# Kernel optimization log

Measured on AMD Instinct MI355X. Metric: run time of the kernel, lower is better.

## Reference

```python
import jax, jax.numpy as jnp
import numpy as np
from jax import lax

D_MODEL = 512
CLASS_NUM = 8000
MAX_LEN = 80
VOCAB = 8002  # len(char2idx): chars + sos/eos
SOS_IDX = 0


def setup_inputs() -> dict:
    key = jax.random.key(0)
    ks = jax.random.split(key, 16)
    T, B, D, V, C = 128, 128, D_MODEL, VOCAB, CLASS_NUM
    s = 1.0 / np.sqrt(D)
    inp = {
        "inputs": jax.random.normal(ks[0], (T, B, D), jnp.float32),
        # additive attention params (query_size=key_size=hidden_size=D)
        "Wq": jax.random.normal(ks[1], (D, D), jnp.float32) * s,
        "bq": jnp.zeros((D,), jnp.float32),
        "Wk": jax.random.normal(ks[2], (D, D), jnp.float32) * s,
        "bk": jnp.zeros((D,), jnp.float32),
        "v": jax.random.normal(ks[3], (D,), jnp.float32) * s,
        # GRUCell: input_size = 2*D, hidden_size = D (PyTorch layout)
        "W_ih": jax.random.normal(ks[4], (3 * D, 2 * D), jnp.float32) * s,
        "b_ih": jnp.zeros((3 * D,), jnp.float32),
        "W_hh": jax.random.normal(ks[5], (3 * D, D), jnp.float32) * s,
        "b_hh": jnp.zeros((3 * D,), jnp.float32),
        # embedding table and classifier
        "emb": jax.random.normal(ks[6], (V, D), jnp.float32),
        "Wc": jax.random.normal(ks[7], (C, D), jnp.float32) * s,
        "bc": jnp.zeros((C,), jnp.float32),
    }
    return inp


def _gru_cell(x, h, W_ih, b_ih, W_hh, b_hh):
    # PyTorch GRUCell math
    gi = x @ W_ih.T + b_ih  # [B, 3D]
    gh = h @ W_hh.T + b_hh  # [B, 3D]
    i_r, i_z, i_n = jnp.split(gi, 3, axis=1)
    h_r, h_z, h_n = jnp.split(gh, 3, axis=1)
    r = jax.nn.sigmoid(i_r + h_r)
    z = jax.nn.sigmoid(i_z + h_z)
    n = jnp.tanh(i_n + r * h_n)
    return (1.0 - z) * n + z * h


def reference(inputs, Wq, bq, Wk, bk, v, W_ih, b_ih, W_hh, b_hh, emb, Wc, bc):
    T, B, D = inputs.shape
    # Attention is called as attention(inputs, keys) with keys = inputs each
    # step -> weights are loop-invariant; compute the context once.
    e = jnp.tanh(inputs @ Wq.T + bq + inputs @ Wk.T + bk) @ v  # [T, B]
    att = jax.nn.softmax(e, axis=0)[..., None]  # [T, B, 1]
    c = jnp.sum(att * inputs, axis=0)  # [B, D]

    h0 = inputs[0]  # initial GRU hidden = first encoder frame
    out0 = emb[jnp.full((B,), SOS_IDX, dtype=jnp.int32)]  # sos embedding

    def step(carry, _):
        h, out = carry
        x = jnp.concatenate([out, c], axis=1)  # [B, 2D]
        h = _gru_cell(x, h, W_ih, b_ih, W_hh, b_hh)
        pred = h @ Wc.T + bc  # [B, class_num]
        top1 = jnp.argmax(pred, axis=1)  # greedy decode (eval mode)
        return (h, emb[top1]), pred

    _, preds = lax.scan(step, (h0, out0), None, length=MAX_LEN)
    return preds  # [max_len, B, class_num]
```

## Files before the change

### kernel.cpp

```cpp
#include <hip/hip_runtime.h>
#include <cstdint>
#include <cstddef>

#define D_MOD 512
#define TH3   1536
#define CLS   8000
#define MAXLEN 80
#define B_SZ  128
#define T_LEN 128
#define NK0   16

typedef __attribute__((ext_vector_type(8))) __bf16 bf16x8;
typedef __attribute__((ext_vector_type(8))) unsigned short u16x8;
typedef __attribute__((ext_vector_type(4))) float f32x4;

__device__ __forceinline__ unsigned short f2bf(float x) {
    unsigned u = __float_as_uint(x);
    unsigned r = ((u >> 16) & 1u) + 0x7fffu;
    return (unsigned short)((u + r) >> 16);
}
__device__ __forceinline__ float bf2f(unsigned short h) {
    return __uint_as_float(((unsigned)h) << 16);
}
__device__ __forceinline__ f32x4 mfma16(u16x8 a, u16x8 b, f32x4 c) {
    return __builtin_amdgcn_mfma_f32_16x16x32_bf16(
        __builtin_bit_cast(bf16x8, a), __builtin_bit_cast(bf16x8, b), c, 0, 0, 0);
}
__device__ __forceinline__ void conv8(const float* __restrict__ p, u16x8& hi, u16x8& lo) {
    float4 f0 = *(const float4*)p;
    float4 f1 = *(const float4*)(p + 4);
    float fs[8] = {f0.x, f0.y, f0.z, f0.w, f1.x, f1.y, f1.z, f1.w};
    #pragma unroll
    for (int j = 0; j < 8; ++j) {
        unsigned short h = f2bf(fs[j]);
        hi[j] = h;
        lo[j] = f2bf(fs[j] - bf2f(h));
    }
}
__device__ __forceinline__ unsigned long long packkey(float v, int n) {
    unsigned u = __float_as_uint(v);
    u = (u & 0x80000000u) ? ~u : (u | 0x80000000u);
    return ((unsigned long long)u << 32) | (unsigned)(~(unsigned)n);
}
__device__ __forceinline__ unsigned long long shfl_xor_u64(unsigned long long x, int mask) {
    unsigned lo = (unsigned)x, hi = (unsigned)(x >> 32);
    lo = __shfl_xor(lo, mask, 16);
    hi = __shfl_xor(hi, mask, 16);
    return ((unsigned long long)hi << 32) | lo;
}
__device__ __forceinline__ size_t pk_off(int n, int k) {
    int tile = n >> 4, lr = n & 15, k0i = k >> 5, lk = (k >> 3) & 3, e = k & 7;
    return ((size_t)(tile * NK0 + k0i) * 64 + (lk * 16 + lr)) * 8 + e;
}

__global__ __launch_bounds__(256) void cvt2p_kernel(
    const float* __restrict__ s1, const float* __restrict__ s2, int ld,
    long total4, unsigned short* __restrict__ hi, unsigned short* __restrict__ lo)
{
    long i4 = (long)blockIdx.x * 256 + threadIdx.x;
    if (i4 >= total4) return;
    long r = i4 >> 7;
    int c = (int)(i4 & 127) * 4;
    float4 a = *(const float4*)(s1 + r * (long)ld + c);
    if (s2) {
        float4 b = *(const float4*)(s2 + r * (long)ld + c);
        a.x += b.x; a.y += b.y; a.z += b.z; a.w += b.w;
    }
    float xs[4] = {a.x, a.y, a.z, a.w};
    unsigned short hs[4], ls[4];
    #pragma unroll
    for (int j = 0; j < 4; ++j) {
        hs[j] = f2bf(xs[j]);
        ls[j] = f2bf(xs[j] - bf2f(hs[j]));
    }
    size_t o = pk_off((int)r, c);
    *(ushort4*)(hi + o) = make_ushort4(hs[0], hs[1], hs[2], hs[3]);
    *(ushort4*)(lo + o) = make_ushort4(ls[0], ls[1], ls[2], ls[3]);
}

template<bool GATHER_CONV, bool CONVB, bool ADD2D, bool ARGMAX, int NS, int KS>
__device__ __forceinline__ void gemm_ks2(
    const unsigned short* __restrict__ Ahi, const unsigned short* __restrict__ Alo,
    const float* __restrict__ Afp, const unsigned long long* __restrict__ gslot,
    const unsigned short* __restrict__ Bhi, const unsigned short* __restrict__ Blo,
    const float* __restrict__ Bfp,
    const float* __restrict__ bias, const float* __restrict__ D2,
    float* __restrict__ C, int ldc,
    unsigned long long* __restrict__ aslot, int bx, int by)
{
    static_assert(NS * KS == 8, "8 waves per block");
    __shared__ float red[(KS - 1) * NS * 576];
    const int tid = threadIdx.x;
    const int w = tid >> 6, lane = tid & 63;
    const int lr = lane & 15, lk = lane >> 4;
    const int ns = w % NS, ks = w / NS;
    const int m0 = by * 16;
    const int n0 = (bx * NS + ns) * 32;
    const int tA = by;
    const int tB0 = n0 >> 4, tB1 = tB0 + 1;

    const float* paf = nullptr;
    if constexpr (GATHER_CONV) {
        int g = (int)(~(unsigned)gslot[m0 + lr]);
        paf = Afp + (size_t)g * D_MOD + lk * 8;
    }
    const float *pb0f = nullptr, *pb1f = nullptr;
    if constexpr (CONVB) {
        pb0f = Bfp + (size_t)(n0 + lr) * D_MOD + lk * 8;
        pb1f = Bfp + (size_t)(n0 + 16 + lr) * D_MOD + lk * 8;
    }

    f32x4 acc0 = (f32x4){0.f, 0.f, 0.f, 0.f};
    f32x4 acc1 = (f32x4){0.f, 0.f, 0.f, 0.f};

    const int kBeg = ks * (NK0 / KS), kEnd = kBeg + (NK0 / KS);
    for (int k0i = kBeg; k0i < kEnd; ++k0i) {
        u16x8 ah, al, b0h, b0l, b1h, b1l;
        if constexpr (GATHER_CONV) {
            conv8(paf + k0i * 32, ah, al);
        } else {
            size_t oA = ((size_t)(tA * NK0 + k0i) * 64 + lane) * 8;
            ah = *(const u16x8*)(Ahi + oA); al = *(const u16x8*)(Alo + oA);
        }
        if constexpr (CONVB) {
            conv8(pb0f + k0i * 32, b0h, b0l);
            conv8(pb1f + k0i * 32, b1h, b1l);
        } else {
            size_t oB0 = ((size_t)(tB0 * NK0 + k0i) * 64 + lane) * 8;
            size_t oB1 = ((size_t)(tB1 * NK0 + k0i) * 64 + lane) * 8;
            b0h = *(const u16x8*)(Bhi + oB0); b0l = *(const u16x8*)(Blo + oB0);
            b1h = *(const u16x8*)(Bhi + oB1); b1l = *(const u16x8*)(Blo + oB1);
        }
        acc0 = mfma16(ah, b0h, acc0);
        acc0 = mfma16(ah, b0l, acc0);
        acc0 = mfma16(al, b0h, acc0);
        acc1 = mfma16(ah, b1h, acc1);
        acc1 = mfma16(ah, b1l, acc1);
        acc1 = mfma16(al, b1h, acc1);
    }

    float af[8];
    #pragma unroll
    for (int i = 0; i < 4; ++i) { af[i] = acc0[i]; af[4 + i] = acc1[i]; }

    if (ks > 0) {
        const int slot = (ks - 1) * NS + ns;
        #pragma unroll
        for (int i = 0; i < 8; ++i) red[slot * 576 + lane * 9 + i] = af[i];
    }
    __syncthreads();
    if (ks == 0) {
        #pragma unroll
        for (int j = 1; j < KS; ++j) {
            const int slot = (j - 1) * NS + ns;
            #pragma unroll
            for (int i = 0; i < 8; ++i) af[i] += red[slot * 576 + lane * 9 + i];
        }
        #pragma unroll
        for (int r = 0; r < 4; ++r) {
            const int row = m0 + lk * 4 + r;
            unsigned long long kmax = 0ull;
            #pragma unroll
            for (int ni = 0; ni < 2; ++ni) {
                const int col = n0 + ni * 16 + lr;
                float val = af[ni * 4 + r];
                if (bias) val += bias[col];
                if constexpr (ADD2D) val += D2[(size_t)row * ldc + col];
                C[(size_t)row * ldc + col] = val;
                if constexpr (ARGMAX) {
                    unsigned long long k = packkey(val, col);
                    if (k > kmax) kmax = k;
                }
            }
            if constexpr (ARGMAX) {
                #pragma unroll
                for (int off = 1; off < 16; off <<= 1) {
                    unsigned long long o = shfl_xor_u64(kmax, off);
                    if (o > kmax) kmax = o;
                }
                if (lr == 0) atomicMax(&aslot[row], kmax);
            }
        }
    }
}

template<int G>
__device__ __forceinline__ bool xcd_map(int p, int& bx, int& by) {
    int x = p & 7, s = p >> 3;
    by = s & 7;
    bx = x * G + (s >> 3);
    return true;
}

__global__ __launch_bounds__(512) void step_dual_kernel(
    const unsigned short* __restrict__ hHi, const unsigned short* __restrict__ hLo,
    const unsigned short* __restrict__ WhhHi, const unsigned short* __restrict__ WhhLo,
    const float* __restrict__ b_hh,
    const float* __restrict__ emb, const unsigned long long* __restrict__ sPrev,
    const unsigned short* __restrict__ WihaHi, const unsigned short* __restrict__ WihaLo,
    const float* __restrict__ gc,
    float* __restrict__ gh, float* __restrict__ gi)
{
    int p = blockIdx.x;
    const int z = (p >= 384);
    p -= z * 384;
    int bx, by;
    xcd_map<6>(p, bx, by);
    if (z == 0)
        gemm_ks2<false, false, false, false, 1, 8>(hHi, hLo, nullptr, nullptr,
            WhhHi, WhhLo, nullptr, b_hh, nullptr, gh, TH3, nullptr, bx, by);
    else
        gemm_ks2<true, false, true, false, 1, 8>(nullptr, nullptr, emb, sPrev,
            WihaHi, WihaLo, nullptr, nullptr, gc, gi, TH3, nullptr, bx, by);
}

__global__ __launch_bounds__(512) void gemm128_kernel(
    const unsigned short* __restrict__ Ahi, const unsigned short* __restrict__ Alo,
    const unsigned short* __restrict__ Bhi, const unsigned short* __restrict__ Blo,
    const float* __restrict__ bias, float* __restrict__ C)
{
    int bx, by;
    xcd_map<6>(blockIdx.x, bx, by);
    gemm_ks2<false, false, false, false, 1, 8>(Ahi, Alo, nullptr, nullptr,
        Bhi, Blo, nullptr, bias, nullptr, C, TH3, nullptr, bx, by);
}

template<bool CONVB>
__global__ __launch_bounds__(512) void cls_kernel(
    const unsigned short* __restrict__ hHi, const unsigned short* __restrict__ hLo,
    const unsigned short* __restrict__ WcHi, const unsigned short* __restrict__ WcLo,
    const float* __restrict__ Wc, const float* __restrict__ bc,
    float* __restrict__ C, unsigned long long* __restrict__ aslot)
{
    int bx, by;
    xcd_map<16>(blockIdx.x, bx, by);
    if (bx >= 125) return;
    gemm_ks2<false, CONVB, false, true, 2, 4>(hHi, hLo, nullptr, nullptr,
        WcHi, WcLo, Wc, bc, nullptr, C, CLS, aslot, bx, by);
}

__global__ __launch_bounds__(256) void attn_e_mfma(
    const float* __restrict__ inp,
    const unsigned short* __restrict__ WqkHi, const unsigned short* __restrict__ WqkLo,
    const float* __restrict__ bq, const float* __restrict__ bk,
    const float* __restrict__ v, float* __restrict__ e)
{
    __shared__ __align__(16) unsigned short Ah[32][40];
    __shared__ __align__(16) unsigned short Al[32][40];
    __shared__ float red[4][32];
    const int tid = threadIdx.x, w = tid >> 6, lane = tid & 63;
    const int lr = lane & 15, lk = lane >> 4;
    const int m0 = blockIdx.x * 32;
    const int srow = tid >> 3, scol = (tid & 7) * 4;

    f32x4 acc[2][8];
    #pragma unroll
    for (int i = 0; i < 2; ++i)
        #pragma unroll
        for (int j = 0; j < 8; ++j) acc[i][j] = (f32x4){0.f, 0.f, 0.f, 0.f};

    for (int k0i = 0; k0i < NK0; ++k0i) {
        float4 x = *(const float4*)(inp + (size_t)(m0 + srow) * D_MOD + k0i * 32 + scol);
        float xs[4] = {x.x, x.y, x.z, x.w};
        #pragma unroll
        for (int j = 0; j < 4; ++j) {
            unsigned short h = f2bf(xs[j]);
            Ah[srow][scol + j] = h;
            Al[srow][scol + j] = f2bf(xs[j] - bf2f(h));
        }
        __syncthreads();
        u16x8 a[2][2];
        #pragma unroll
        for (int mi = 0; mi < 2; ++mi) {
            a[mi][0] = *(const u16x8*)&Ah[mi * 16 + lr][lk * 8];
            a[mi][1] = *(const u16x8*)&Al[mi * 16 + lr][lk * 8];
        }
        #pragma unroll
        for (int nf = 0; nf < 8; ++nf) {
            const int tile = w * 8 + nf;
            size_t ob = ((size_t)(tile * NK0 + k0i) * 64 + lane) * 8;
            u16x8 bh = *(const u16x8*)(WqkHi + ob);
            u16x8 bl = *(const u16x8*)(WqkLo + ob);
            #pragma unroll
            for (int mi = 0; mi < 2; ++mi) {
                acc[mi][nf] = mfma16(a[mi][0], bh, acc[mi][nf]);
                acc[mi][nf] = mfma16(a[mi][0], bl, acc[mi][nf]);
                acc[mi][nf] = mfma16(a[mi][1], bh, acc[mi][nf]);
            }
        }
        __syncthreads();
    }

    float ep[2][4];
    #pragma unroll
    for (int mi = 0; mi < 2; ++mi)
        #pragma unroll
        for (int r = 0; r < 4; ++r) ep[mi][r] = 0.f;
    #pragma unroll
    for (int nf = 0; nf < 8; ++nf) {
        const int col = w * 128 + nf * 16 + lr;
        const float bb = bq[col] + bk[col];
        const float vv = v[col];
        #pragma unroll
        for (int mi = 0; mi < 2; ++mi)
            #pragma unroll
            for (int r = 0; r < 4; ++r)
                ep[mi][r] += vv * tanhf(acc[mi][nf][r] + bb);
    }
    #pragma unroll
    for (int mi = 0; mi < 2; ++mi)
        #pragma unroll
        for (int r = 0; r < 4; ++r) {
            float s = ep[mi][r];
            #pragma unroll
            for (int off = 1; off < 16; off <<= 1) s += __shfl_xor(s, off, 16);
            if (lr == 0) red[w][mi * 16 + lk * 4 + r] = s;
        }
    __syncthreads();
    if (tid < 32) e[m0 + tid] = red[0][tid] + red[1][tid] + red[2][tid] + red[3][tid];
}

__global__ __launch_bounds__(256) void softmax_ctx_kernel(
    const float* __restrict__ inp, const float* __restrict__ e,
    unsigned short* __restrict__ cHi, unsigned short* __restrict__ cLo,
    float* __restrict__ h1, unsigned short* __restrict__ h1Hi, unsigned short* __restrict__ h1Lo,
    unsigned long long* __restrict__ slots)
{
    __shared__ float att[T_LEN];
    __shared__ float red;
    const int b = blockIdx.x, tid = threadIdx.x;
    float val = -1e30f;
    if (tid < T_LEN) { val = e[(size_t)tid * B_SZ + b]; att[tid] = val; }
    __syncthreads();
    if (tid < 64) {
        float m = fmaxf(att[tid], att[tid + 64]);
        #pragma unroll
        for (int off = 32; off; off >>= 1) m = fmaxf(m, __shfl_xor(m, off));
        if (tid == 0) red = m;
    }
    __syncthreads();
    const float mx = red;
    __syncthreads();
    if (tid < T_LEN) att[tid] = expf(val - mx);
    __syncthreads();
    if (tid < 64) {
        float s = att[tid] + att[tid + 64];
        #pragma unroll
        for (int off = 32; off; off >>= 1) s += __shfl_xor(s, off);
        if (tid == 0) red = s;
    }
    __syncthreads();
    const float inv = 1.f / red;

    const int d0 = tid * 2;
    float ax = 0.f, ay = 0.f;
    for (int t = 0; t < T_LEN; ++t) {
        float a = att[t];
        float2 x = *(const float2*)(inp + ((size_t)t * B_SZ + b) * D_MOD + d0);
        ax += a * x.x; ay += a * x.y;
        if (t == 0) {
            *(float2*)(h1 + (size_t)b * D_MOD + d0) = x;
            unsigned short hx = f2bf(x.x), hy = f2bf(x.y);
            h1Hi[pk_off(b, d0)]     = hx;
            h1Hi[pk_off(b, d0 + 1)] = hy;
            h1Lo[pk_off(b, d0)]     = f2bf(x.x - bf2f(hx));
            h1Lo[pk_off(b, d0 + 1)] = f2bf(x.y - bf2f(hy));
        }
    }
    ax *= inv; ay *= inv;
    unsigned short cx = f2bf(ax), cy = f2bf(ay);
    cHi[pk_off(b, d0)]     = cx;
    cHi[pk_off(b, d0 + 1)] = cy;
    cLo[pk_off(b, d0)]     = f2bf(ax - bf2f(cx));
    cLo[pk_off(b, d0 + 1)] = f2bf(ay - bf2f(cy));
    if (tid == 0) {
        slots[b] = 0ull;
        slots[B_SZ + b] = 0x00000000FFFFFFFFull;
    }
}

__global__ __launch_bounds__(512) void gru_combine(
    const float* __restrict__ gh, const float* __restrict__ gi,
    const float* __restrict__ hPrev, float* __restrict__ hCur,
    unsigned short* __restrict__ hHiC, unsigned short* __restrict__ hLoC,
    unsigned long long* __restrict__ slotCur)
{
    const int b = blockIdx.x, k = threadIdx.x;
    const float* gib = gi + (size_t)b * TH3;
    const float* ghb = gh + (size_t)b * TH3;
    float r = 1.f / (1.f + expf(-(gib[k] + ghb[k])));
    float z = 1.f / (1.f + expf(-(gib[k + 512] + ghb[k + 512])));
    float n = tanhf(gib[k + 1024] + r * ghb[k + 1024]);
    float h = hPrev[(size_t)b * D_MOD + k];
    float hv = (1.f - z) * n + z * h;
    hCur[(size_t)b * D_MOD + k] = hv;
    unsigned short hh = f2bf(hv);
    size_t o = pk_off(b, k);
    hHiC[o] = hh;
    hLoC[o] = f2bf(hv - bf2f(hh));
    if (k == 0) slotCur[b] = 0ull;
}

extern "C" void kernel_launch(void* const* d_in, const int* in_sizes, int n_in,
                              void* d_out, int out_size, void* d_ws, size_t ws_size,
                              hipStream_t stream)
{
    const float* inp  = (const float*)d_in[0];
    const float* Wq   = (const float*)d_in[1];
    const float* bq   = (const float*)d_in[2];
    const float* Wk   = (const float*)d_in[3];
    const float* bk   = (const float*)d_in[4];
    const float* v    = (const float*)d_in[5];
    const float* W_ih = (const float*)d_in[6];
    const float* b_ih = (const float*)d_in[7];
    const float* W_hh = (const float*)d_in[8];
    const float* b_hh = (const float*)d_in[9];
    const float* emb  = (const float*)d_in[10];
    const float* Wc   = (const float*)d_in[11];
    const float* bc   = (const float*)d_in[12];
    float* out = (float*)d_out;

    char* base = (char*)d_ws;
    size_t off = 0;
    auto alloc = [&](size_t bytes) -> char* {
        char* q = base + off;
        off += (bytes + 255) & ~(size_t)255;
        return q;
    };
    typedef unsigned short us;
    us* WqkHi  = (us*)alloc(512 * 512 * 2);
    us* WqkLo  = (us*)alloc(512 * 512 * 2);
    us* WhhHi  = (us*)alloc((size_t)TH3 * 512 * 2);
    us* WhhLo  = (us*)alloc((size_t)TH3 * 512 * 2);
    us* WihaHi = (us*)alloc((size_t)TH3 * 512 * 2);
    us* WihaLo = (us*)alloc((size_t)TH3 * 512 * 2);
    us* WihbHi = (us*)alloc((size_t)TH3 * 512 * 2);
    us* WihbLo = (us*)alloc((size_t)TH3 * 512 * 2);
    float* e   = (float*)alloc(T_LEN * B_SZ * 4);
    us* cHi    = (us*)alloc(B_SZ * 512 * 2);
    us* cLo    = (us*)alloc(B_SZ * 512 * 2);
    float* gc  = (float*)alloc((size_t)B_SZ * TH3 * 4);
    float* gh  = (float*)alloc((size_t)B_SZ * TH3 * 4);
    float* gi  = (float*)alloc((size_t)B_SZ * TH3 * 4);
    float* hF[2]; us* hHi[2]; us* hLo[2];
    hF[0] = (float*)alloc(B_SZ * 512 * 4);
    hF[1] = (float*)alloc(B_SZ * 512 * 4);
    hHi[0] = (us*)alloc(B_SZ * 512 * 2);
    hHi[1] = (us*)alloc(B_SZ * 512 * 2);
    hLo[0] = (us*)alloc(B_SZ * 512 * 2);
    hLo[1] = (us*)alloc(B_SZ * 512 * 2);
    unsigned long long* slots = (unsigned long long*)alloc(2 * B_SZ * 8);
    us* WcHi = (us*)alloc((size_t)CLS * 512 * 2);
    us* WcLo = (us*)alloc((size_t)CLS * 512 * 2);
    const bool PREB = (off <= ws_size);

    cvt2p_kernel<<<(512 * 128) / 256, 256, 0, stream>>>(Wq, Wk, 512, 512L * 128, WqkHi, WqkLo);
    cvt2p_kernel<<<(TH3 * 128) / 256, 256, 0, stream>>>(W_hh, nullptr, 512, (long)TH3 * 128, WhhHi, WhhLo);
    cvt2p_kernel<<<(TH3 * 128) / 256, 256, 0, stream>>>(W_ih, nullptr, 1024, (long)TH3 * 128, WihaHi, WihaLo);
    cvt2p_kernel<<<(TH3 * 128) / 256, 256, 0, stream>>>(W_ih + 512, nullptr, 1024, (long)TH3 * 128, WihbHi, WihbLo);
    if (PREB)
        cvt2p_kernel<<<(CLS * 128) / 256, 256, 0, stream>>>(Wc, nullptr, 512, (long)CLS * 128, WcHi, WcLo);

    attn_e_mfma<<<(T_LEN * B_SZ) / 32, 256, 0, stream>>>(inp, WqkHi, WqkLo, bq, bk, v, e);
    softmax_ctx_kernel<<<B_SZ, 256, 0, stream>>>(inp, e, cHi, cLo, hF[1], hHi[1], hLo[1], slots);
    gemm128_kernel<<<384, 512, 0, stream>>>(cHi, cLo, WihbHi, WihbLo, b_ih, gc);

    for (int t = 0; t < MAXLEN; ++t) {
        const int pi = (t + 1) & 1, ci = t & 1;
        unsigned long long* sPrev = slots + pi * B_SZ;
        unsigned long long* sCur  = slots + ci * B_SZ;

        step_dual_kernel<<<768, 512, 0, stream>>>(
            hHi[pi], hLo[pi], WhhHi, WhhLo, b_hh,
            emb, sPrev, WihaHi, WihaLo, gc, gh, gi);
        gru_combine<<<B_SZ, 512, 0, stream>>>(
            gh, gi, hF[pi], hF[ci], hHi[ci], hLo[ci], sCur);
        if (PREB)
            cls_kernel<false><<<1024, 512, 0, stream>>>(
                hHi[ci], hLo[ci], WcHi, WcLo, nullptr, bc,
                out + (size_t)t * B_SZ * CLS, sCur);
        else
            cls_kernel<true><<<1024, 512, 0, stream>>>(
                hHi[ci], hLo[ci], nullptr, nullptr, Wc, bc,
                out + (size_t)t * B_SZ * CLS, sCur);
    }
}
```

Before: 2.986 ms.

## Precompute embedding input-gate table and fuse GRU combine into hidden GEMM

Greedy decoding only ever feeds embedding rows into the W_ih input half, so the code now computes emb @ W_ih_a once for all 8000 class rows before the loop. Each step then gathers the needed row instead of running a per-step gathered GEMM. The per-step gh GEMM kernel also absorbs the GRU elementwise update: the last 32 blocks to finish, detected with an atomic counter, spin until every block is done and then compute the new hidden state, which removes one launch per step. The trade-offs are a large one-time GEMM with a big fp32 table, and a grid-wide spin-wait that relies on all blocks being resident at the same time.

Result: slower. 4.045 ms (+35.5%).

```diff
diff --git a/kernel.cpp b/kernel.cpp
--- a/kernel.cpp
+++ b/kernel.cpp
@@ -9,6 +9,7 @@
 #define B_SZ  128
 #define T_LEN 128
 #define NK0   16
+#define EGI_ROWS 8000
 
 typedef __attribute__((ext_vector_type(8))) __bf16 bf16x8;
 typedef __attribute__((ext_vector_type(8))) unsigned short u16x8;
@@ -101,7 +102,7 @@
 
     const float* paf = nullptr;
     if constexpr (GATHER_CONV) {
-        int g = (int)(~(unsigned)gslot[m0 + lr]);
+        int g = gslot ? (int)(~(unsigned)gslot[m0 + lr]) : (m0 + lr);
         paf = Afp + (size_t)g * D_MOD + lk * 8;
     }
     const float *pb0f = nullptr, *pb1f = nullptr;
@@ -192,26 +193,80 @@
     return true;
 }
 
-__global__ __launch_bounds__(512) void step_dual_kernel(
+__global__ __launch_bounds__(512) void egi_kernel(
+    const float* __restrict__ emb,
+    const unsigned short* __restrict__ WihaHi, const unsigned short* __restrict__ WihaLo,
+    float* __restrict__ Egi)
+{
+    int p = blockIdx.x;
+    int x = p & 7, s = p >> 3;
+    int by = s % 500, bx = x * 6 + s / 500;
+    gemm_ks2<true, false, false, false, 1, 8>(nullptr, nullptr, emb, nullptr,
+        WihaHi, WihaLo, nullptr, nullptr, nullptr, Egi, TH3, nullptr, bx, by);
+}
+
+#define N1_BLOCKS 384
+#define N1_TAILS  32
+#define N1_ROWS   4
+__global__ __launch_bounds__(512) void gh_gru_kernel(
     const unsigned short* __restrict__ hHi, const unsigned short* __restrict__ hLo,
     const unsigned short* __restrict__ WhhHi, const unsigned short* __restrict__ WhhLo,
-    const float* __restrict__ b_hh,
-    const float* __restrict__ emb, const unsigned long long* __restrict__ sPrev,
-    const unsigned short* __restrict__ WihaHi, const unsigned short* __restrict__ WihaLo,
-    const float* __restrict__ gc,
-    float* __restrict__ gh, float* __restrict__ gi)
-{
-    int p = blockIdx.x;
-    const int z = (p >= 384);
-    p -= z * 384;
+    const float* __restrict__ b_hh, float* __restrict__ gh,
+    const float* __restrict__ Egi, const float* __restrict__ gc,
+    const unsigned long long* __restrict__ sPrev,
+    const float* __restrict__ hPrevF, float* __restrict__ hCurF,
+    unsigned short* __restrict__ hHiC, unsigned short* __restrict__ hLoC,
+    unsigned long long* __restrict__ slotCur,
+    unsigned* __restrict__ ctr)
+{
     int bx, by;
-    xcd_map<6>(p, bx, by);
-    if (z == 0)
-        gemm_ks2<false, false, false, false, 1, 8>(hHi, hLo, nullptr, nullptr,
-            WhhHi, WhhLo, nullptr, b_hh, nullptr, gh, TH3, nullptr, bx, by);
-    else
-        gemm_ks2<true, false, true, false, 1, 8>(nullptr, nullptr, emb, sPrev,
-            WihaHi, WihaLo, nullptr, nullptr, gc, gi, TH3, nullptr, bx, by);
+    xcd_map<6>(blockIdx.x, bx, by);
+    gemm_ks2<false, false, false, false, 1, 8>(hHi, hLo, nullptr, nullptr,
+        WhhHi, WhhLo, nullptr, b_hh, nullptr, gh, TH3, nullptr, bx, by);
+
+    __shared__ unsigned tk_sh;
+    const int tid = threadIdx.x;
+    __syncthreads();
+    if (tid == 0) {
+        __threadfence();
+        tk_sh = atomicAdd(ctr, 1u);
+    }
+    __syncthreads();
+    const unsigned tk = tk_sh;
+    if (tk < (unsigned)(N1_BLOCKS - N1_TAILS)) return;
+
+    if (tid == 0) {
+        while (__hip_atomic_load(ctr, __ATOMIC_RELAXED, __HIP_MEMORY_SCOPE_AGENT)
+               < (unsigned)N1_BLOCKS)
+            __builtin_amdgcn_s_sleep(4);
+        __threadfence();
+    }
+    __syncthreads();
+
+    const int k = tid;
+    const int r0 = (int)(tk - (unsigned)(N1_BLOCKS - N1_TAILS)) * N1_ROWS;
+    #pragma unroll
+    for (int i = 0; i < N1_ROWS; ++i) {
+        const int b = r0 + i;
+        const int sel = (int)(~(unsigned)sPrev[b]);
+        const float* gib = Egi + (size_t)sel * TH3;
+        const float* gcb = gc + (size_t)b * TH3;
+        const float* ghb = gh + (size_t)b * TH3;
+        float gi0 = gib[k] + gcb[k];
+        float gi1 = gib[k + 512] + gcb[k + 512];
+        float gi2 = gib[k + 1024] + gcb[k + 1024];
+        float r = 1.f / (1.f + expf(-(gi0 + ghb[k])));
+        float z = 1.f / (1.f + expf(-(gi1 + ghb[k + 512])));
+        float n = tanhf(gi2 + r * ghb[k + 1024]);
+        float h = hPrevF[(size_t)b * D_MOD + k];
+        float hv = (1.f - z) * n + z * h;
+        hCurF[(size_t)b * D_MOD + k] = hv;
+        unsigned short hh = f2bf(hv);
+        size_t o = pk_off(b, k);
+        hHiC[o] = hh;
+        hLoC[o] = f2bf(hv - bf2f(hh));
+        if (k == 0) slotCur[b] = 0ull;
+    }
 }
 
 __global__ __launch_bounds__(512) void gemm128_kernel(
@@ -324,11 +379,12 @@
     const float* __restrict__ inp, const float* __restrict__ e,
     unsigned short* __restrict__ cHi, unsigned short* __restrict__ cLo,
     float* __restrict__ h1, unsigned short* __restrict__ h1Hi, unsigned short* __restrict__ h1Lo,
-    unsigned long long* __restrict__ slots)
+    unsigned long long* __restrict__ slots, unsigned* __restrict__ ctrs)
 {
     __shared__ float att[T_LEN];
     __shared__ float red;
     const int b = blockIdx.x, tid = threadIdx.x;
+    if (b == 0 && tid < MAXLEN) ctrs[tid] = 0u;
     float val = -1e30f;
     if (tid < T_LEN) { val = e[(size_t)tid * B_SZ + b]; att[tid] = val; }
     __syncthreads();
@@ -377,28 +433,6 @@
         slots[b] = 0ull;
         slots[B_SZ + b] = 0x00000000FFFFFFFFull;
     }
-}
-
-__global__ __launch_bounds__(512) void gru_combine(
-    const float* __restrict__ gh, const float* __restrict__ gi,
-    const float* __restrict__ hPrev, float* __restrict__ hCur,
-    unsigned short* __restrict__ hHiC, unsigned short* __restrict__ hLoC,
-    unsigned long long* __restrict__ slotCur)
-{
-    const int b = blockIdx.x, k = threadIdx.x;
-    const float* gib = gi + (size_t)b * TH3;
-    const float* ghb = gh + (size_t)b * TH3;
-    float r = 1.f / (1.f + expf(-(gib[k] + ghb[k])));
-    float z = 1.f / (1.f + expf(-(gib[k + 512] + ghb[k + 512])));
-    float n = tanhf(gib[k + 1024] + r * ghb[k + 1024]);
-    float h = hPrev[(size_t)b * D_MOD + k];
-    float hv = (1.f - z) * n + z * h;
-    hCur[(size_t)b * D_MOD + k] = hv;
-    unsigned short hh = f2bf(hv);
-    size_t o = pk_off(b, k);
-    hHiC[o] = hh;
-    hLoC[o] = f2bf(hv - bf2f(hh));
-    if (k == 0) slotCur[b] = 0ull;
 }
 
 extern "C" void kernel_launch(void* const* d_in, const int* in_sizes, int n_in,
@@ -441,7 +475,8 @@
     us* cLo    = (us*)alloc(B_SZ * 512 * 2);
     float* gc  = (float*)alloc((size_t)B_SZ * TH3 * 4);
     float* gh  = (float*)alloc((size_t)B_SZ * TH3 * 4);
-    float* gi  = (float*)alloc((size_t)B_SZ * TH3 * 4);
+    float* Egi = (float*)alloc((size_t)EGI_ROWS * TH3 * 4);
+    unsigned* ctrs = (unsigned*)alloc(MAXLEN * 4);
     float* hF[2]; us* hHi[2]; us* hLo[2];
     hF[0] = (float*)alloc(B_SZ * 512 * 4);
     hF[1] = (float*)alloc(B_SZ * 512 * 4);
@@ -461,8 +496,10 @@
     if (PREB)
         cvt2p_kernel<<<(CLS * 128) / 256, 256, 0, stream>>>(Wc, nullptr, 512, (long)CLS * 128, WcHi, WcLo);
 
+    egi_kernel<<<8 * 6 * 500, 512, 0, stream>>>(emb, WihaHi, WihaLo, Egi);
+
     attn_e_mfma<<<(T_LEN * B_SZ) / 32, 256, 0, stream>>>(inp, WqkHi, WqkLo, bq, bk, v, e);
-    softmax_ctx_kernel<<<B_SZ, 256, 0, stream>>>(inp, e, cHi, cLo, hF[1], hHi[1], hLo[1], slots);
+    softmax_ctx_kernel<<<B_SZ, 256, 0, stream>>>(inp, e, cHi, cLo, hF[1], hHi[1], hLo[1], slots, ctrs);
     gemm128_kernel<<<384, 512, 0, stream>>>(cHi, cLo, WihbHi, WihbLo, b_ih, gc);
 
     for (int t = 0; t < MAXLEN; ++t) {
@@ -470,11 +507,11 @@
         unsigned long long* sPrev = slots + pi * B_SZ;
         unsigned long long* sCur  = slots + ci * B_SZ;
 
-        step_dual_kernel<<<768, 512, 0, stream>>>(
-            hHi[pi], hLo[pi], WhhHi, WhhLo, b_hh,
-            emb, sPrev, WihaHi, WihaLo, gc, gh, gi);
-        gru_combine<<<B_SZ, 512, 0, stream>>>(
-            gh, gi, hF[pi], hF[ci], hHi[ci], hLo[ci], sCur);
+        gh_gru_kernel<<<N1_BLOCKS, 512, 0, stream>>>(
+            hHi[pi], hLo[pi], WhhHi, WhhLo, b_hh, gh,
+            Egi, gc, sPrev,
+            hF[pi], hF[ci], hHi[ci], hLo[ci], sCur,
+            ctrs + t);
         if (PREB)
             cls_kernel<false><<<1024, 512, 0, stream>>>(
                 hHi[ci], hLo[ci], WcHi, WcLo, nullptr, bc,
```

## Precompute embedding-times-W_ih table and gather input gates per decode step

Applied to the files above, without the earlier changes.

Before the decode loop, a new kernel precomputes emb @ W_ih[:, :D]^T for all 8000 class rows. Each step then runs only the hidden-state GEMM (gh_kernel), and the combine kernel gathers the input-gate row for the previous argmax token and adds the context-gate term. This removes the per-step gather-and-convert input GEMM, so each step launches half as many GEMM blocks. In exchange it adds a large one-time GEMM every call and a table of roughly 49 MB of workspace, and falls back to the old path if the workspace is too small.

Measured after the change: 2.945 ms. No clear change (-1.4%).

```diff
diff --git a/kernel.cpp b/kernel.cpp
--- a/kernel.cpp
+++ b/kernel.cpp
@@ -9,6 +9,7 @@
 #define B_SZ  128
 #define T_LEN 128
 #define NK0   16
+#define EGI_ROWS 8000
 
 typedef __attribute__((ext_vector_type(8))) __bf16 bf16x8;
 typedef __attribute__((ext_vector_type(8))) unsigned short u16x8;
@@ -101,7 +102,7 @@
 
     const float* paf = nullptr;
     if constexpr (GATHER_CONV) {
-        int g = (int)(~(unsigned)gslot[m0 + lr]);
+        int g = gslot ? (int)(~(unsigned)gslot[m0 + lr]) : (m0 + lr);
         paf = Afp + (size_t)g * D_MOD + lk * 8;
     }
     const float *pb0f = nullptr, *pb1f = nullptr;
@@ -192,6 +193,29 @@
     return true;
 }
 
+__global__ __launch_bounds__(512) void egi_kernel(
+    const float* __restrict__ emb,
+    const unsigned short* __restrict__ WihaHi, const unsigned short* __restrict__ WihaLo,
+    float* __restrict__ Egi)
+{
+    int p = blockIdx.x;
+    int x = p & 7, s = p >> 3;
+    int by = s % 500, bx = x * 6 + s / 500;
+    gemm_ks2<true, false, false, false, 1, 8>(nullptr, nullptr, emb, nullptr,
+        WihaHi, WihaLo, nullptr, nullptr, nullptr, Egi, TH3, nullptr, bx, by);
+}
+
+__global__ __launch_bounds__(512) void gh_kernel(
+    const unsigned short* __restrict__ hHi, const unsigned short* __restrict__ hLo,
+    const unsigned short* __restrict__ WhhHi, const unsigned short* __restrict__ WhhLo,
+    const float* __restrict__ b_hh, float* __restrict__ gh)
+{
+    int bx, by;
+    xcd_map<6>(blockIdx.x, bx, by);
+    gemm_ks2<false, false, false, false, 1, 8>(hHi, hLo, nullptr, nullptr,
+        WhhHi, WhhLo, nullptr, b_hh, nullptr, gh, TH3, nullptr, bx, by);
+}
+
 __global__ __launch_bounds__(512) void step_dual_kernel(
     const unsigned short* __restrict__ hHi, const unsigned short* __restrict__ hLo,
     const unsigned short* __restrict__ WhhHi, const unsigned short* __restrict__ WhhLo,
@@ -391,6 +415,34 @@
     float r = 1.f / (1.f + expf(-(gib[k] + ghb[k])));
     float z = 1.f / (1.f + expf(-(gib[k + 512] + ghb[k + 512])));
     float n = tanhf(gib[k + 1024] + r * ghb[k + 1024]);
+    float h = hPrev[(size_t)b * D_MOD + k];
+    float hv = (1.f - z) * n + z * h;
+    hCur[(size_t)b * D_MOD + k] = hv;
+    unsigned short hh = f2bf(hv);
+    size_t o = pk_off(b, k);
+    hHiC[o] = hh;
+    hLoC[o] = f2bf(hv - bf2f(hh));
+    if (k == 0) slotCur[b] = 0ull;
+}
+
+__global__ __launch_bounds__(512) void gru_combine_egi(
+    const float* __restrict__ gh, const float* __restrict__ Egi,
+    const float* __restrict__ gc, const unsigned long long* __restrict__ sPrev,
+    const float* __restrict__ hPrev, float* __restrict__ hCur,
+    unsigned short* __restrict__ hHiC, unsigned short* __restrict__ hLoC,
+    unsigned long long* __restrict__ slotCur)
+{
+    const int b = blockIdx.x, k = threadIdx.x;
+    const int sel = (int)(~(unsigned)sPrev[b]);
+    const float* gib = Egi + (size_t)sel * TH3;
+    const float* gcb = gc + (size_t)b * TH3;
+    const float* ghb = gh + (size_t)b * TH3;
+    float gi0 = gib[k] + gcb[k];
+    float gi1 = gib[k + 512] + gcb[k + 512];
+    float gi2 = gib[k + 1024] + gcb[k + 1024];
+    float r = 1.f / (1.f + expf(-(gi0 + ghb[k])));
+    float z = 1.f / (1.f + expf(-(gi1 + ghb[k + 512])));
+    float n = tanhf(gi2 + r * ghb[k + 1024]);
     float h = hPrev[(size_t)b * D_MOD + k];
     float hv = (1.f - z) * n + z * h;
     hCur[(size_t)b * D_MOD + k] = hv;
@@ -453,6 +505,8 @@
     us* WcHi = (us*)alloc((size_t)CLS * 512 * 2);
     us* WcLo = (us*)alloc((size_t)CLS * 512 * 2);
     const bool PREB = (off <= ws_size);
+    float* Egi = (float*)alloc((size_t)EGI_ROWS * TH3 * 4);
+    const bool EGIB = (off <= ws_size);
 
     cvt2p_kernel<<<(512 * 128) / 256, 256, 0, stream>>>(Wq, Wk, 512, 512L * 128, WqkHi, WqkLo);
     cvt2p_kernel<<<(TH3 * 128) / 256, 256, 0, stream>>>(W_hh, nullptr, 512, (long)TH3 * 128, WhhHi, WhhLo);
@@ -460,6 +514,8 @@
     cvt2p_kernel<<<(TH3 * 128) / 256, 256, 0, stream>>>(W_ih + 512, nullptr, 1024, (long)TH3 * 128, WihbHi, WihbLo);
     if (PREB)
         cvt2p_kernel<<<(CLS * 128) / 256, 256, 0, stream>>>(Wc, nullptr, 512, (long)CLS * 128, WcHi, WcLo);
+    if (EGIB)
+        egi_kernel<<<8 * 6 * 500, 512, 0, stream>>>(emb, WihaHi, WihaLo, Egi);
 
     attn_e_mfma<<<(T_LEN * B_SZ) / 32, 256, 0, stream>>>(inp, WqkHi, WqkLo, bq, bk, v, e);
     softmax_ctx_kernel<<<B_SZ, 256, 0, stream>>>(inp, e, cHi, cLo, hF[1], hHi[1], hLo[1], slots);
@@ -470,11 +526,18 @@
         unsigned long long* sPrev = slots + pi * B_SZ;
         unsigned long long* sCur  = slots + ci * B_SZ;
 
-        step_dual_kernel<<<768, 512, 0, stream>>>(
-            hHi[pi], hLo[pi], WhhHi, WhhLo, b_hh,
-            emb, sPrev, WihaHi, WihaLo, gc, gh, gi);
-        gru_combine<<<B_SZ, 512, 0, stream>>>(
-            gh, gi, hF[pi], hF[ci], hHi[ci], hLo[ci], sCur);
+        if (EGIB) {
+            gh_kernel<<<384, 512, 0, stream>>>(
+                hHi[pi], hLo[pi], WhhHi, WhhLo, b_hh, gh);
+            gru_combine_egi<<<B_SZ, 512, 0, stream>>>(
+                gh, Egi, gc, sPrev, hF[pi], hF[ci], hHi[ci], hLo[ci], sCur);
+        } else {
+            step_dual_kernel<<<768, 512, 0, stream>>>(
+                hHi[pi], hLo[pi], WhhHi, WhhLo, b_hh,
+                emb, sPrev, WihaHi, WihaLo, gc, gh, gi);
+            gru_combine<<<B_SZ, 512, 0, stream>>>(
+                gh, gi, hF[pi], hF[ci], hHi[ci], hLo[ci], sCur);
+        }
         if (PREB)
             cls_kernel<false><<<1024, 512, 0, stream>>>(
                 hHi[ci], hLo[ci], WcHi, WcLo, nullptr, bc,
```
